# Kernel optimization log

Hardware: AMD Instinct MI355X
Metric: run time of the kernel (lower is better)

Reference implementation:

```python
import jax, jax.numpy as jnp
import numpy as np

NH, HD, WS, LL, SR, HF = 8, 32, 3, 9, 8, 682


def _ln(x, w, b, eps=1e-5):
    m = x.mean(-1, keepdims=True)
    v = ((x - m) ** 2).mean(-1, keepdims=True)
    return (x - m) * jax.lax.rsqrt(v + eps) * w + b


def _l2norm(x, eps=1e-12):
    n = jnp.sqrt(jnp.sum(x * x, axis=-1, keepdims=True))
    return x / jnp.maximum(n, eps)


def setup_inputs() -> dict:
    key = jax.random.key(0)
    ks = jax.random.split(key, 32)
    f32 = jnp.float32
    rn = lambda i, shp, s=0.02: jax.random.normal(ks[i], shp, f32) * s
    B, N, C, T = 8, 3136, 256, 1024
    d = {}
    d['x'] = jax.random.normal(ks[0], (B, N, C), f32)
    d['relative_coords_table'] = jax.random.uniform(ks[1], (T, 2), f32, minval=-1.0, maxval=1.0)
    d['seq_length_scale'] = jnp.ones((1,), f32)
    d['norm1_w'] = jnp.ones((C,), f32); d['norm1_b'] = jnp.zeros((C,), f32)
    d['q_w'] = rn(2, (C, C)); d['q_b'] = rn(3, (C,))
    d['kv_w'] = rn(4, (2 * C, C)); d['kv_b'] = rn(5, (2 * C,))
    d['temperature'] = jnp.full((NH, 1, 1), np.log(np.expm1(1.0 / 0.24)), f32)
    d['query_embedding'] = rn(6, (NH, 1, HD))
    d['relative_pos_bias_local'] = rn(7, (NH, LL), 0.0004)
    d['learnable_tokens'] = rn(8, (NH, HD, LL))
    d['learnable_bias'] = jnp.zeros((NH, 1, LL), f32)
    d['sr_w'] = rn(9, (C, C)); d['sr_b'] = rn(10, (C,))
    d['normp_w'] = jnp.ones((C,), f32); d['normp_b'] = jnp.zeros((C,), f32)
    d['cpb_fc1_w'] = rn(11, (512, 2)); d['cpb_fc1_b'] = rn(12, (512,))
    d['cpb_fc2_w'] = rn(13, (NH, 512)); d['cpb_fc2_b'] = rn(14, (NH,))
    d['proj_w'] = rn(15, (C, C)); d['proj_b'] = rn(16, (C,))
    d['norm2_w'] = jnp.ones((C,), f32); d['norm2_b'] = jnp.zeros((C,), f32)
    d['fc1_w'] = rn(17, (2 * HF, C)); d['fc1_b'] = rn(18, (2 * HF,))
    d['dw_w'] = rn(19, (HF, 1, 3, 3)); d['dw_b'] = rn(20, (HF,))
    d['fc2_w'] = rn(21, (C, HF)); d['fc2_b'] = rn(22, (C,))
    d['relative_pos_index'] = jax.random.randint(ks[23], (N, 49), 0, T)
    d['padding_mask'] = jnp.zeros((N, LL), bool)
    d['H'] = 56
    d['W'] = 56
    return d


def _forward(x, relative_coords_table, seq_length_scale, norm1_w, norm1_b, q_w, q_b, kv_w, kv_b,
             temperature, query_embedding, relative_pos_bias_local, learnable_tokens, learnable_bias,
             sr_w, sr_b, normp_w, normp_b, cpb_fc1_w, cpb_fc1_b, cpb_fc2_w, cpb_fc2_b,
             proj_w, proj_b, norm2_w, norm2_b, fc1_w, fc1_b, dw_w, dw_b, fc2_w, fc2_b,
             relative_pos_index, padding_mask, H, W):
    B, N, C = x.shape
    pH, pW = H // SR, W // SR
    pl = pH * pW
    xn = _ln(x, norm1_w, norm1_b)
    # queries: [B, nh, N, hd], cosine-normalized
    q = (xn @ q_w.T + q_b).reshape(B, N, NH, HD).transpose(0, 2, 1, 3)
    q_norm = _l2norm(q)
    q_scaled = (q_norm + query_embedding) * jax.nn.softplus(temperature) * seq_length_scale
    # local keys/values via unfold (3x3 windows, zero-padded)
    kv = xn @ kv_w.T + kv_b                                   # [B, N, 2C]
    k_l, v_l = jnp.split(kv, 2, axis=-1)
    k_l = _l2norm(k_l.reshape(B, N, NH, HD)).reshape(B, N, C)
    kvl = jnp.concatenate([k_l, v_l], -1).transpose(0, 2, 1).reshape(B, 2 * C, H, W)
    pad = WS // 2
    kvp = jnp.pad(kvl, ((0, 0), (0, 0), (pad, pad), (pad, pad)))
    wins = jnp.stack([kvp[:, :, i:i + H, j:j + W] for i in range(WS) for j in range(WS)], axis=2)
    wins = wins.reshape(B, 2 * NH, HD, LL, N).transpose(0, 1, 4, 2, 3)  # [B, 2nh, N, hd, ll]
    k_loc, v_loc = jnp.split(wins, 2, axis=1)
    attn_local = jnp.einsum('bhnd,bhndl->bhnl', q_scaled, k_loc) + relative_pos_bias_local[None, :, None, :]
    attn_local = jnp.where(padding_mask[None, None], -jnp.inf, attn_local)
    # pooled global branch
    x_ = xn.transpose(0, 2, 1).reshape(B, C, H, W)
    x_ = jax.nn.gelu(jnp.einsum('oc,bchw->bohw', sr_w, x_) + sr_b[None, :, None, None], approximate=False)
    x_ = x_.reshape(B, C, pH, SR, pW, SR).mean(axis=(3, 5))  # adaptive avg pool
    x_ = _ln(x_.reshape(B, C, pl).transpose(0, 2, 1), normp_w, normp_b)
    kvp2 = (x_ @ kv_w.T + kv_b).reshape(B, pl, 2 * NH, HD).transpose(0, 2, 1, 3)
    k_pool, v_pool = jnp.split(kvp2, 2, axis=1)               # [B, nh, pl, hd]
    cpb = jax.nn.relu(relative_coords_table @ cpb_fc1_w.T + cpb_fc1_b) @ cpb_fc2_w.T + cpb_fc2_b
    pool_bias = cpb.T[:, relative_pos_index.reshape(-1)].reshape(NH, N, pl)
    attn_pool = q_scaled @ _l2norm(k_pool).transpose(0, 1, 3, 2) + pool_bias[None]
    # joint softmax over local + pool scores
    attn = jax.nn.softmax(jnp.concatenate([attn_local, attn_pool], -1), axis=-1)
    a_loc, a_pool = attn[..., :LL], attn[..., LL:]
    x_local = jnp.einsum('bhnl,bhndl->bhnd',
                         jnp.einsum('bhnd,hdl->bhnl', q_norm, learnable_tokens) + learnable_bias[None] + a_loc,
                         v_loc)
    x_pool = a_pool @ v_pool
    out = (x_local + x_pool).transpose(0, 2, 1, 3).reshape(B, N, C)
    x = x + (out @ proj_w.T + proj_b)
    # ConvolutionalGLU MLP
    xn2 = _ln(x, norm2_w, norm2_b)
    h = xn2 @ fc1_w.T + fc1_b
    h1, v = jnp.split(h, 2, -1)
    hc = h1.transpose(0, 2, 1).reshape(B, HF, H, W)
    hc = jax.lax.conv_general_dilated(hc, dw_w, (1, 1), 'SAME', feature_group_count=HF,
                                      dimension_numbers=('NCHW', 'OIHW', 'NCHW')) + dw_b[None, :, None, None]
    h1 = hc.reshape(B, HF, N).transpose(0, 2, 1)
    h = jax.nn.gelu(h1, approximate=False) * v
    return x + (h @ fc2_w.T + fc2_b)


def reference(x, relative_coords_table, seq_length_scale, norm1_w, norm1_b, q_w, q_b, kv_w, kv_b,
              temperature, query_embedding, relative_pos_bias_local, learnable_tokens, learnable_bias,
              sr_w, sr_b, normp_w, normp_b, cpb_fc1_w, cpb_fc1_b, cpb_fc2_w, cpb_fc2_b,
              proj_w, proj_b, norm2_w, norm2_b, fc1_w, fc1_b, dw_w, dw_b, fc2_w, fc2_b,
              relative_pos_index, padding_mask, H, W):
    return _forward(x, relative_coords_table, seq_length_scale, norm1_w, norm1_b, q_w, q_b, kv_w, kv_b,
                    temperature, query_embedding, relative_pos_bias_local, learnable_tokens, learnable_bias,
                    sr_w, sr_b, normp_w, normp_b, cpb_fc1_w, cpb_fc1_b, cpb_fc2_w, cpb_fc2_b,
                    proj_w, proj_b, norm2_w, norm2_b, fc1_w, fc1_b, dw_w, dw_b, fc2_w, fc2_b,
                    relative_pos_index, padding_mask, H, W)
```

## Files before the change

kernel.cpp:

```cpp
#include <hip/hip_runtime.h>
#include <math.h>

#define B_   8
#define N_   3136
#define C_   256
#define NH_  8
#define HD_  32
#define LL_  9
#define PL_  49
#define HF_  682
#define HH   56
#define WW   56
#define MROWS (B_*N_)
#define HGLD  704
#define F2LD  704
#define HBLD  1368

typedef short          bf16x8 __attribute__((ext_vector_type(8)));
typedef unsigned short u16x8  __attribute__((ext_vector_type(8)));
typedef float          f32x4  __attribute__((ext_vector_type(4)));
typedef unsigned short u16;

static __device__ __forceinline__ float gelu_f(float x){ return 0.5f*x*(1.0f+erff(x*0.70710678118654752f)); }
static __device__ __forceinline__ u16 f2bf(float f){
  union { float f; unsigned u; } x; x.f = f;
  unsigned r = (x.u + 0x7FFFu + ((x.u >> 16) & 1u)) >> 16;
  return (u16)r;
}
static __device__ __forceinline__ float b2f(u16 u){
  union { unsigned u; float f; } x; x.u = ((unsigned)u) << 16;
  return x.f;
}
static __device__ __forceinline__ void gld_lds16(const u16* g, u16* l){
  __builtin_amdgcn_global_load_lds((const __attribute__((address_space(1))) void*)g,
                                   (__attribute__((address_space(3))) void*)l, 16, 0, 0);
}
static __device__ __forceinline__ float rsum32(float v){
  #pragma unroll
  for (int m=16;m>0;m>>=1) v += __shfl_xor(v,m,32);
  return v;
}
static __device__ __forceinline__ float rsum64(float v){
  #pragma unroll
  for (int m=32;m>0;m>>=1) v += __shfl_xor(v,m,64);
  return v;
}
static __device__ __forceinline__ float rsum8(float v){
  v += __shfl_xor(v,1,64);
  v += __shfl_xor(v,2,64);
  v += __shfl_xor(v,4,64);
  return v;
}

__global__ __launch_bounds__(256) void cvt_all(const float* __restrict__ q_w,
                                               const float* __restrict__ kv_w,
                                               const float* __restrict__ sr_w,
                                               const float* __restrict__ pw,
                                               const float* __restrict__ f1w,
                                               const float* __restrict__ f2w,
                                               const float* __restrict__ lt,
                                               const float* __restrict__ dww,
                                               u16* __restrict__ wq,
                                               u16* __restrict__ wkv,
                                               u16* __restrict__ wsr,
                                               u16* __restrict__ wp,
                                               u16* __restrict__ wf1,
                                               u16* __restrict__ wf2,
                                               u16* __restrict__ w72,
                                               float* __restrict__ dwwT){
  int t = blockIdx.x*256 + threadIdx.x;
  int seg = blockIdx.y;
  const int NT = 64*256;
  if (seg == 0){
    float4 v = *(const float4*)(q_w + (size_t)t*4);
    ushort4 o; o.x=f2bf(v.x); o.y=f2bf(v.y); o.z=f2bf(v.z); o.w=f2bf(v.w);
    *(ushort4*)(wq + (size_t)t*4) = o;
  } else if (seg == 1){
    for (int i=t; i<32768; i+=NT){
      float4 v = *(const float4*)(kv_w + (size_t)i*4);
      ushort4 o; o.x=f2bf(v.x); o.y=f2bf(v.y); o.z=f2bf(v.z); o.w=f2bf(v.w);
      *(ushort4*)(wkv + (size_t)i*4) = o;
    }
  } else if (seg == 2){
    float4 v = *(const float4*)(sr_w + (size_t)t*4);
    ushort4 o; o.x=f2bf(v.x); o.y=f2bf(v.y); o.z=f2bf(v.z); o.w=f2bf(v.w);
    *(ushort4*)(wsr + (size_t)t*4) = o;
  } else if (seg == 3){
    float4 v = *(const float4*)(pw + (size_t)t*4);
    ushort4 o; o.x=f2bf(v.x); o.y=f2bf(v.y); o.z=f2bf(v.z); o.w=f2bf(v.w);
    *(ushort4*)(wp + (size_t)t*4) = o;
  } else if (seg == 4){
    for (int i=t; i<360448; i+=NT){
      int r = i >> 8;
      wf1[i] = (r < 1364) ? f2bf(f1w[i]) : (u16)0;
    }
  } else if (seg == 5){
    for (int i=t; i<256*F2LD; i+=NT){
      int r = i/F2LD, k = i - r*F2LD;
      wf2[i] = (k < HF_) ? f2bf(f2w[(size_t)r*HF_ + k]) : (u16)0;
    }
  } else if (seg == 6){
    for (int i=t; i<72*256; i+=NT){
      int r = i >> 8, c = i & 255;
      int h = r/9, l = r - h*9;
      w72[i] = ((c>>5) == h) ? f2bf(lt[((size_t)(h*32 + (c&31)))*9 + l]) : (u16)0;
    }
  } else {
    for (int i=t; i<9*684; i+=NT){
      int l = i/684, f = i - l*684;
      dwwT[i] = (f < HF_) ? dww[(size_t)f*9 + l] : 0.f;
    }
  }
}

__global__ __launch_bounds__(256) void ln4_kernel(const float* __restrict__ in,
                                                  const float* __restrict__ w,
                                                  const float* __restrict__ bsh,
                                                  u16* __restrict__ out){
  int t = threadIdx.x, wv = t>>6, l = t&63;
  int row = blockIdx.x*4 + wv;
  const float* rp = in + (size_t)row*C_ + l*4;
  float4 v = *(const float4*)rp;
  float s = v.x+v.y+v.z+v.w;
  float q = v.x*v.x+v.y*v.y+v.z*v.z+v.w*v.w;
  s = rsum64(s); q = rsum64(q);
  float m = s*(1.0f/C_);
  float var = q*(1.0f/C_)-m*m;
  float inv = rsqrtf(var+1e-5f);
  float4 wvv = *(const float4*)(w + l*4);
  float4 bvv = *(const float4*)(bsh + l*4);
  ushort4 o;
  o.x = f2bf((v.x-m)*inv*wvv.x + bvv.x);
  o.y = f2bf((v.y-m)*inv*wvv.y + bvv.y);
  o.z = f2bf((v.z-m)*inv*wvv.z + bvv.z);
  o.w = f2bf((v.w-m)*inv*wvv.w + bvv.w);
  *(ushort4*)(out + (size_t)row*C_ + l*4) = o;
}

template<int ACT, int RES, int OUTBF>
__global__ __launch_bounds__(256) void gemm64b(const u16* __restrict__ A, int lda,
                                               const u16* __restrict__ W, int ldw,
                                               const float* __restrict__ bias,
                                               const float* __restrict__ res,
                                               void* __restrict__ outv,
                                               int M, int Nt, int K){
  constexpr int LDT = 40;
  __shared__ u16 As[64*LDT];
  __shared__ u16 Bs[64*LDT];
  int tid = threadIdx.x, lane = tid & 63;
  int wave = tid >> 6;
  int m0 = blockIdx.x*64, n0 = blockIdx.y*64;
  int wm = (wave>>1)*32, wn = (wave&1)*32;
  f32x4 acc[2][2];
  #pragma unroll
  for (int i=0;i<2;i++)
    #pragma unroll
    for (int j=0;j<2;j++) acc[i][j] = (f32x4){0.f,0.f,0.f,0.f};

  const int Kt = (K + 31) & ~31;
  const int l15 = lane & 15, quad = lane >> 4;
  int r  = tid >> 2;
  int c8 = (tid & 3) * 8;

  for (int k0=0; k0<Kt; k0+=32){
    int gk = k0 + c8;
    u16x8 av = (u16x8){0,0,0,0,0,0,0,0};
    if (m0 + r < M && gk + 8 <= lda)
      av = *(const u16x8*)(A + (size_t)(m0+r)*lda + gk);
    *(u16x8*)(&As[r*LDT + c8]) = av;
    u16x8 bv = (u16x8){0,0,0,0,0,0,0,0};
    if (n0 + r < Nt && gk + 8 <= ldw)
      bv = *(const u16x8*)(W + (size_t)(n0+r)*ldw + gk);
    *(u16x8*)(&Bs[r*LDT + c8]) = bv;
    __syncthreads();
    bf16x8 af[2], bfr[2];
    #pragma unroll
    for (int mi=0;mi<2;mi++)
      af[mi] = *(bf16x8*)(&As[(wm + mi*16 + l15)*LDT + quad*8]);
    #pragma unroll
    for (int nj=0;nj<2;nj++)
      bfr[nj] = *(bf16x8*)(&Bs[(wn + nj*16 + l15)*LDT + quad*8]);
    #pragma unroll
    for (int mi=0;mi<2;mi++)
      #pragma unroll
      for (int nj=0;nj<2;nj++)
        acc[mi][nj] = __builtin_amdgcn_mfma_f32_16x16x32_bf16(af[mi], bfr[nj], acc[mi][nj], 0,0,0);
    __syncthreads();
  }
  int rbase = quad*4;
  #pragma unroll
  for (int nj=0;nj<2;nj++){
    int gc = n0 + wn + nj*16 + l15;
    if (gc >= Nt) continue;
    float bv = bias[gc];
    #pragma unroll
    for (int mi=0;mi<2;mi++){
      #pragma unroll
      for (int reg=0;reg<4;reg++){
        int gr = m0 + wm + mi*16 + rbase + reg;
        if (gr >= M) continue;
        float v = acc[mi][nj][reg] + bv;
        if (ACT==1) v = gelu_f(v);
        if (RES)   v += res[(size_t)gr*Nt + gc];
        if (OUTBF) ((u16*)outv)[(size_t)gr*Nt + gc] = f2bf(v);
        else       ((float*)outv)[(size_t)gr*Nt + gc] = v;
      }
    }
  }
}

__global__ __launch_bounds__(256) void gemm64r(const u16* __restrict__ A, int lda,
                                               const u16* __restrict__ W, int ldw,
                                               const float* __restrict__ bias,
                                               const float* __restrict__ res,
                                               float* __restrict__ outv,
                                               int Nt, int Kt){
  constexpr int LDT = 40;
  __shared__ u16 As[64*LDT];
  __shared__ u16 Bs[64*LDT];
  int tid = threadIdx.x, lane = tid & 63;
  int wave = tid >> 6;
  int m0 = blockIdx.x*64, n0 = blockIdx.y*64;
  int wm = (wave>>1)*32, wn = (wave&1)*32;
  f32x4 acc[2][2];
  #pragma unroll
  for (int i=0;i<2;i++)
    #pragma unroll
    for (int j=0;j<2;j++) acc[i][j] = (f32x4){0.f,0.f,0.f,0.f};

  const int l15 = lane & 15, quad = lane >> 4;
  int r  = tid >> 2;
  int c8 = (tid & 3) * 8;
  const u16* ga = A + (size_t)(m0+r)*lda + c8;
  const u16* gb = W + (size_t)(n0+r)*ldw + c8;

  for (int k0=0; k0<Kt; k0+=32){
    *(u16x8*)(&As[r*LDT + c8]) = *(const u16x8*)(ga + k0);
    *(u16x8*)(&Bs[r*LDT + c8]) = *(const u16x8*)(gb + k0);
    __syncthreads();
    bf16x8 af[2], bfr[2];
    #pragma unroll
    for (int mi=0;mi<2;mi++)
      af[mi] = *(bf16x8*)(&As[(wm + mi*16 + l15)*LDT + quad*8]);
    #pragma unroll
    for (int nj=0;nj<2;nj++)
      bfr[nj] = *(bf16x8*)(&Bs[(wn + nj*16 + l15)*LDT + quad*8]);
    #pragma unroll
    for (int mi=0;mi<2;mi++)
      #pragma unroll
      for (int nj=0;nj<2;nj++)
        acc[mi][nj] = __builtin_amdgcn_mfma_f32_16x16x32_bf16(af[mi], bfr[nj], acc[mi][nj], 0,0,0);
    __syncthreads();
  }
  int rbase = quad*4;
  #pragma unroll
  for (int nj=0;nj<2;nj++){
    int gc = n0 + wn + nj*16 + l15;
    float bv = bias[gc];
    #pragma unroll
    for (int mi=0;mi<2;mi++){
      #pragma unroll
      for (int reg=0;reg<4;reg++){
        int gr = m0 + wm + mi*16 + rbase + reg;
        outv[(size_t)gr*Nt + gc] = acc[mi][nj][reg] + bv + res[(size_t)gr*Nt + gc];
      }
    }
  }
}

__global__ __launch_bounds__(256) void gemm64f(const u16* __restrict__ A,
                                               const u16* __restrict__ W0,
                                               const u16* __restrict__ W1,
                                               const u16* __restrict__ W2,
                                               const float* __restrict__ b0,
                                               const float* __restrict__ b1,
                                               const float* __restrict__ b2,
                                               u16* __restrict__ o0,
                                               u16* __restrict__ o1,
                                               u16* __restrict__ o2){
  constexpr int LDT = 40;
  __shared__ u16 As[64*LDT];
  __shared__ u16 Bs[64*LDT];
  int tid = threadIdx.x, lane = tid & 63;
  int wave = tid >> 6;
  int m0 = blockIdx.x*64, y = blockIdx.y;
  const u16* Wp; const float* bp; u16* dst; int dld, dcol0; bool act = false;
  if (y < 4)      { Wp = W0 + (size_t)y*64*C_;      bp = b0 + y*64;      dst = o0; dld = 256; dcol0 = y*64; }
  else if (y < 12){ Wp = W1 + (size_t)(y-4)*64*C_;  bp = b1 + (y-4)*64;  dst = o1; dld = 512; dcol0 = (y-4)*64; }
  else            { Wp = W2 + (size_t)(y-12)*64*C_; bp = b2 + (y-12)*64; dst = o2; dld = 256; dcol0 = (y-12)*64; act = true; }
  int wm = (wave>>1)*32, wn = (wave&1)*32;
  f32x4 acc[2][2];
  #pragma unroll
  for (int i=0;i<2;i++)
    #pragma unroll
    for (int j=0;j<2;j++) acc[i][j] = (f32x4){0.f,0.f,0.f,0.f};

  const int l15 = lane & 15, quad = lane >> 4;
  int r  = tid >> 2;
  int c8 = (tid & 3) * 8;

  #pragma unroll 1
  for (int k0=0; k0<256; k0+=32){
    int gk = k0 + c8;
    *(u16x8*)(&As[r*LDT + c8]) = *(const u16x8*)(A  + (size_t)(m0+r)*C_ + gk);
    *(u16x8*)(&Bs[r*LDT + c8]) = *(const u16x8*)(Wp + (size_t)r*C_ + gk);
    __syncthreads();
    bf16x8 af[2], bfr[2];
    #pragma unroll
    for (int mi=0;mi<2;mi++)
      af[mi] = *(bf16x8*)(&As[(wm + mi*16 + l15)*LDT + quad*8]);
    #pragma unroll
    for (int nj=0;nj<2;nj++)
      bfr[nj] = *(bf16x8*)(&Bs[(wn + nj*16 + l15)*LDT + quad*8]);
    #pragma unroll
    for (int mi=0;mi<2;mi++)
      #pragma unroll
      for (int nj=0;nj<2;nj++)
        acc[mi][nj] = __builtin_amdgcn_mfma_f32_16x16x32_bf16(af[mi], bfr[nj], acc[mi][nj], 0,0,0);
    __syncthreads();
  }
  int rbase = quad*4;
  #pragma unroll
  for (int nj=0;nj<2;nj++){
    int cc = wn + nj*16 + l15;
    float bv = bp[cc];
    #pragma unroll
    for (int mi=0;mi<2;mi++){
      #pragma unroll
      for (int reg=0;reg<4;reg++){
        int gr = m0 + wm + mi*16 + rbase + reg;
        float v = acc[mi][nj][reg] + bv;
        if (act) v = gelu_f(v);
        dst[(size_t)gr*dld + dcol0 + cc] = f2bf(v);
      }
    }
  }
}

template<int EPI>
__global__ __launch_bounds__(256) void gemm128t(const u16* __restrict__ A, int lda,
                                                const u16* __restrict__ W0,
                                                const float* __restrict__ b0,
                                                u16* __restrict__ o0,
                                                int M, int Nt, int K, int ldo){
  __shared__ u16 smem[8704];
  u16* As = smem;
  u16* Bs = smem + 4096;
  int tid = threadIdx.x, lane = tid & 63, wave = tid >> 6;
  int m0 = blockIdx.x*128, y = blockIdx.y;
  int wm = (wave>>1)*64, wn = (wave&1)*64;
  int l15 = lane & 15, quad = lane >> 4;

  const u16* Wp = W0 + (size_t)y*128*(size_t)lda;
  const float* bp = b0;
  u16* dstb = o0; int dld = ldo, dcol0 = y*128;

  f32x4 acc[4][4];
  #pragma unroll
  for (int i=0;i<4;i++)
    #pragma unroll
    for (int j=0;j<4;j++) acc[i][j] = (f32x4){0.f,0.f,0.f,0.f};

  const int Kt = (K + 31) & ~31;
  const u16* ga = A  + (size_t)(m0 + lane)*lda + wave*8;
  const u16* gb = Wp + (size_t)lane*lda + wave*8;
  u16* la = As + wave*1024;
  u16* lb = Bs + wave*1024;

  for (int k0=0; k0<Kt; k0+=32){
    gld_lds16(ga + k0,            la);
    gld_lds16(ga + 64*lda + k0,   la + 512);
    gld_lds16(gb + k0,            lb);
    gld_lds16(gb + 64*lda + k0,   lb + 512);
    __syncthreads();
    bf16x8 af[4], bfr[4];
    #pragma unroll
    for (int mi=0;mi<4;mi++)
      af[mi] = *(bf16x8*)(&As[quad*1024 + (wm + mi*16 + l15)*8]);
    #pragma unroll
    for (int nj=0;nj<4;nj++)
      bfr[nj] = *(bf16x8*)(&Bs[quad*1024 + (wn + nj*16 + l15)*8]);
    #pragma unroll
    for (int mi=0;mi<4;mi++)
      #pragma unroll
      for (int nj=0;nj<4;nj++)
        acc[mi][nj] = __builtin_amdgcn_mfma_f32_16x16x32_bf16(af[mi], bfr[nj], acc[mi][nj], 0,0,0);
    __syncthreads();
  }

  u16* Cs = smem;
  #pragma unroll
  for (int p=0;p<2;p++){
    if (wm == p*64){
      #pragma unroll
      for (int nj=0;nj<4;nj++){
        int cc = wn + nj*16 + l15;
        int gc = dcol0 + cc;
        float bv = (gc < Nt) ? bp[gc] : 0.f;
        #pragma unroll
        for (int mi=0;mi<4;mi++){
          #pragma unroll
          for (int reg=0;reg<4;reg++){
            int rr = mi*16 + quad*4 + reg;
            Cs[rr*136 + cc] = f2bf(acc[mi][nj][reg] + bv);
          }
        }
      }
    }
    __syncthreads();
    int r = tid >> 2, cb = (tid & 3)*32;
    int gr = m0 + p*64 + r;
    if (gr < M){
      u16* op = dstb + (size_t)gr*dld + dcol0;
      #pragma unroll
      for (int k=0;k<4;k++){
        int c0 = cb + k*8;
        if (dcol0 + c0 + 8 <= ldo)
          *(u16x8*)(op + c0) = *(u16x8*)&Cs[r*136 + c0];
      }
    }
    __syncthreads();
  }
}

__global__ __launch_bounds__(256) void post1_kernel(u16* __restrict__ q,
                                                    const float* __restrict__ qe,
                                                    const float* __restrict__ temp,
                                                    const float* __restrict__ sls,
                                                    u16* __restrict__ qs_out,
                                                    u16* __restrict__ kv,
                                                    const u16* __restrict__ xsr,
                                                    const float* __restrict__ npw,
                                                    const float* __restrict__ npb,
                                                    u16* __restrict__ xpln){
  __shared__ float s1[4], s2[4];
  int bid = blockIdx.x, tid = threadIdx.x;
  if (bid < MROWS/4){
    int wv = tid>>6, l = tid&63;
    int row = bid*4 + wv;
    int c = l*4, h = l>>3;
    size_t idx = (size_t)row*C_ + c;
    ushort4 qv = *(const ushort4*)(q + idx);
    float v0=b2f(qv.x), v1=b2f(qv.y), v2=b2f(qv.z), v3=b2f(qv.w);
    float ss = rsum8(v0*v0+v1*v1+v2*v2+v3*v3);
    float inv = 1.0f / fmaxf(sqrtf(ss), 1e-12f);
    float qn0=v0*inv, qn1=v1*inv, qn2=v2*inv, qn3=v3*inv;
    ushort4 qo; qo.x=f2bf(qn0); qo.y=f2bf(qn1); qo.z=f2bf(qn2); qo.w=f2bf(qn3);
    *(ushort4*)(q + idx) = qo;
    float t  = temp[h];
    float sp = log1pf(expf(t));
    float scale = sp * sls[0];
    float4 qev = *(const float4*)(qe + c);
    ushort4 so;
    so.x = f2bf((qn0 + qev.x)*scale);
    so.y = f2bf((qn1 + qev.y)*scale);
    so.z = f2bf((qn2 + qev.z)*scale);
    so.w = f2bf((qn3 + qev.w)*scale);
    *(ushort4*)(qs_out + idx) = so;
    size_t kidx = (size_t)row*512 + c;
    ushort4 kvv = *(const ushort4*)(kv + kidx);
    float k0=b2f(kvv.x), k1=b2f(kvv.y), k2=b2f(kvv.z), k3=b2f(kvv.w);
    float ks = rsum8(k0*k0+k1*k1+k2*k2+k3*k3);
    float kinv = 1.0f / fmaxf(sqrtf(ks), 1e-12f);
    ushort4 ko; ko.x=f2bf(k0*kinv); ko.y=f2bf(k1*kinv); ko.z=f2bf(k2*kinv); ko.w=f2bf(k3*kinv);
    *(ushort4*)(kv + kidx) = ko;
  } else {
    int blk = bid - MROWS/4;
    int b = blk/PL_; int p = blk%PL_;
    int py = p/7, px = p%7;
    int o = tid;
    float s = 0.f;
    for (int iy=0;iy<8;iy++){
      const u16* rowp = xsr + ((size_t)(b*N_ + (py*8+iy)*WW + px*8))*C_ + o;
      #pragma unroll
      for (int ix=0;ix<8;ix++) s += b2f(rowp[(size_t)ix*C_]);
    }
    s *= (1.0f/64.0f);
    float su = rsum64(s), sq = rsum64(s*s);
    if ((o&63)==0){ s1[o>>6]=su; s2[o>>6]=sq; }
    __syncthreads();
    float ts=s1[0]+s1[1]+s1[2]+s1[3];
    float tq=s2[0]+s2[1]+s2[2]+s2[3];
    float m = ts*(1.0f/256.0f), var = tq*(1.0f/256.0f)-m*m;
    float inv = rsqrtf(var+1e-5f);
    xpln[(size_t)blk*C_+o] = f2bf((s-m)*inv*npw[o]+npb[o]);
  }
}

__global__ __launch_bounds__(256) void misc2_kernel(u16* __restrict__ kvp2,
                                                    const float* __restrict__ rct,
                                                    const float* __restrict__ w1,
                                                    const float* __restrict__ b1,
                                                    const float* __restrict__ w2,
                                                    const float* __restrict__ b2v,
                                                    float* __restrict__ cpb){
  __shared__ float r[512];
  int bid = blockIdx.x, tid = threadIdx.x;
  if (bid < B_*PL_){
    int row = bid;
    size_t idx = (size_t)row*512 + tid;
    float v = b2f(kvp2[idx]);
    float ss = rsum32(v*v);
    kvp2[idx] = f2bf(v / fmaxf(sqrtf(ss), 1e-12f));
  } else {
    int t = bid - B_*PL_;
    float c0 = rct[t*2], c1 = rct[t*2+1];
    for (int j=tid;j<512;j+=256){
      float v = c0*w1[j*2] + c1*w1[j*2+1] + b1[j];
      r[j] = fmaxf(v, 0.f);
    }
    __syncthreads();
    int h = tid>>5, lane = tid&31;
    float s = 0.f;
    for (int j=lane;j<512;j+=32) s += r[j]*w2[h*512+j];
    s = rsum32(s);
    if (lane==0) cpb[t*8+h] = s + b2v[h];
  }
}

__global__ __launch_bounds__(256) void attn_all(const u16* __restrict__ qbuf,
                                                const u16* __restrict__ w72,
                                                const float* __restrict__ lb,
                                                float* __restrict__ qlt,
                                                const u16* __restrict__ qs,
                                                const u16* __restrict__ kv,
                                                const float* __restrict__ rpb,
                                                const u16* __restrict__ kvp2,
                                                const float* __restrict__ cpb,
                                                const int* __restrict__ ridx,
                                                float* __restrict__ attn){
  constexpr int LDT = 40;
  __shared__ u16 As[64*LDT];
  __shared__ u16 Bs[64*LDT];
  int bid = blockIdx.x, tid = threadIdx.x;
  int lane = tid & 63, wave = tid >> 6;
  int l15 = lane & 15, quad = lane >> 4;
  if (bid < 784){
    int m0 = (bid % 392)*64, n0 = (bid / 392)*64;
    int wm = (wave>>1)*32, wn = (wave&1)*32;
    f32x4 acc[2][2];
    #pragma unroll
    for (int i=0;i<2;i++)
      #pragma unroll
      for (int j=0;j<2;j++) acc[i][j] = (f32x4){0.f,0.f,0.f,0.f};
    int r  = tid >> 2;
    int c8 = (tid & 3) * 8;
    for (int k0=0; k0<256; k0+=32){
      int gk = k0 + c8;
      *(u16x8*)(&As[r*LDT + c8]) = *(const u16x8*)(qbuf + (size_t)(m0+r)*C_ + gk);
      u16x8 bv = (u16x8){0,0,0,0,0,0,0,0};
      if (n0 + r < 72)
        bv = *(const u16x8*)(w72 + (size_t)(n0+r)*C_ + gk);
      *(u16x8*)(&Bs[r*LDT + c8]) = bv;
      __syncthreads();
      bf16x8 af[2], bfr[2];
      #pragma unroll
      for (int mi=0;mi<2;mi++)
        af[mi] = *(bf16x8*)(&As[(wm + mi*16 + l15)*LDT + quad*8]);
      #pragma unroll
      for (int nj=0;nj<2;nj++)
        bfr[nj] = *(bf16x8*)(&Bs[(wn + nj*16 + l15)*LDT + quad*8]);
      #pragma unroll
      for (int mi=0;mi<2;mi++)
        #pragma unroll
        for (int nj=0;nj<2;nj++)
          acc[mi][nj] = __builtin_amdgcn_mfma_f32_16x16x32_bf16(af[mi], bfr[nj], acc[mi][nj], 0,0,0);
      __syncthreads();
    }
    int rbase = quad*4;
    #pragma unroll
    for (int nj=0;nj<2;nj++){
      int gc = n0 + wn + nj*16 + l15;
      if (gc >= 72) continue;
      float bv = lb[gc];
      #pragma unroll
      for (int mi=0;mi<2;mi++){
        #pragma unroll
        for (int reg=0;reg<4;reg++){
          int gr = m0 + wm + mi*16 + rbase + reg;
          qlt[(size_t)gr*72 + gc] = acc[mi][nj][reg] + bv;
        }
      }
    }
  } else if (bid < 1568){
    int t = tid;
    int row = (bid-784)*32 + (t>>3);
    int h = t & 7;
    int b = row / N_, n = row - b*N_;
    int y = n / WW, x = n - y*WW;
    const u16* qp = qs + (size_t)row*C_ + h*32;
    float q[32];
    #pragma unroll
    for (int j=0;j<4;j++){
      u16x8 v = *(const u16x8*)(qp + j*8);
      #pragma unroll
      for (int e=0;e<8;e++) q[j*8+e] = b2f(v[e]);
    }
    float* arow = attn + ((size_t)row*8 + h)*58;
    #pragma unroll
    for (int l=0;l<9;l++){
      int yy = y + l/3 - 1, xx = x + l%3 - 1;
      float s = 0.f;
      if (yy>=0 && yy<HH && xx>=0 && xx<WW){
        const u16* kp = kv + ((size_t)(b*N_ + yy*WW + xx))*512 + h*32;
        #pragma unroll
        for (int j=0;j<4;j++){
          u16x8 kw = *(const u16x8*)(kp + j*8);
          #pragma unroll
          for (int e=0;e<8;e++) s = fmaf(q[j*8+e], b2f(kw[e]), s);
        }
      }
      arow[l] = s + rpb[h*9+l];
    }
  } else {
    int t = bid - 1568;
    int xblk = t % 49, bh = t / 49;
    int b = bh >> 3, h = bh & 7;
    int n0 = (xblk*4 + wave)*16;
    bf16x8 af = *(const bf16x8*)(qs + ((size_t)(b*N_ + n0 + l15)*C_ + h*32 + quad*8));
    f32x4 acc[4];
    #pragma unroll
    for (int nj=0;nj<4;nj++){
      int p = nj*16 + l15;
      bf16x8 bfr = (bf16x8){0,0,0,0,0,0,0,0};
      if (p < PL_)
        bfr = *(const bf16x8*)(kvp2 + ((size_t)(b*PL_ + p)*512 + h*32 + quad*8));
      f32x4 z = (f32x4){0.f,0.f,0.f,0.f};
      acc[nj] = __builtin_amdgcn_mfma_f32_16x16x32_bf16(af, bfr, z, 0,0,0);
    }
    #pragma unroll
    for (int nj=0;nj<4;nj++){
      int p = nj*16 + l15;
      if (p >= PL_) continue;
      #pragma unroll
      for (int reg=0;reg<4;reg++){
        int n = n0 + quad*4 + reg;
        float bias = cpb[ridx[(size_t)n*PL_ + p]*8 + h];
        attn[((size_t)(b*N_ + n)*8 + h)*58 + 9 + p] = acc[nj][reg] + bias;
      }
    }
  }
}

__global__ __launch_bounds__(256) void xout_v4(const float* __restrict__ qlt,
                                               const float* __restrict__ attn,
                                               const u16* __restrict__ kv,
                                               const u16* __restrict__ kvp2,
                                               u16* __restrict__ out){
  __shared__ float coef[4][472];
  int t = threadIdx.x, w = t>>6, l = t&63;
  int row = blockIdx.x*4 + w;
  int b = row / N_, n = row - b*N_;
  int y = n / WW, x = n - y*WW;
  const float* arow = attn + (size_t)row*464;
  for (int i=l; i<464; i+=64) coef[w][i] = arow[i];
  __syncthreads();
  int h = l>>3, k = l&7;
  float* ch = &coef[w][h*58];
  float e[8];
  float mx = -1e30f;
  #pragma unroll
  for (int i=0;i<8;i++){
    int j = k + i*8;
    e[i] = (j<58) ? ch[j] : -1e30f;
    mx = fmaxf(mx, e[i]);
  }
  mx = fmaxf(mx, __shfl_xor(mx,1,64));
  mx = fmaxf(mx, __shfl_xor(mx,2,64));
  mx = fmaxf(mx, __shfl_xor(mx,4,64));
  float s = 0.f;
  #pragma unroll
  for (int i=0;i<8;i++){
    int j = k + i*8;
    if (j<58){ e[i] = expf(e[i]-mx); s += e[i]; }
  }
  s += __shfl_xor(s,1,64);
  s += __shfl_xor(s,2,64);
  s += __shfl_xor(s,4,64);
  float inv = 1.f/s;
  #pragma unroll
  for (int i=0;i<8;i++){
    int j = k + i*8;
    if (j<58){
      float v = e[i]*inv;
      if (j<9) v += qlt[(size_t)row*72 + h*9 + j];
      ch[j] = v;
    }
  }
  __syncthreads();
  int c = l*4;
  float a0=0.f, a1=0.f, a2=0.f, a3=0.f;
  #pragma unroll
  for (int lw=0; lw<9; lw++){
    int yy = y + lw/3 - 1, xx = x + lw%3 - 1;
    if (yy>=0 && yy<HH && xx>=0 && xx<WW){
      ushort4 vv = *(const ushort4*)(kv + ((size_t)(b*N_ + yy*WW + xx))*512 + 256 + c);
      float cf = ch[lw];
      a0 = fmaf(cf, b2f(vv.x), a0);
      a1 = fmaf(cf, b2f(vv.y), a1);
      a2 = fmaf(cf, b2f(vv.z), a2);
      a3 = fmaf(cf, b2f(vv.w), a3);
    }
  }
  const u16* pb = kvp2 + (size_t)b*PL_*512 + 256 + c;
  #pragma unroll 7
  for (int p=0;p<49;p++){
    ushort4 vv = *(const ushort4*)(pb + (size_t)p*512);
    float cf = ch[9+p];
    a0 = fmaf(cf, b2f(vv.x), a0);
    a1 = fmaf(cf, b2f(vv.y), a1);
    a2 = fmaf(cf, b2f(vv.z), a2);
    a3 = fmaf(cf, b2f(vv.w), a3);
  }
  ushort4 o; o.x=f2bf(a0); o.y=f2bf(a1); o.z=f2bf(a2); o.w=f2bf(a3);
  *(ushort4*)(out + (size_t)row*C_ + c) = o;
}

__global__ __launch_bounds__(256) void dwconv_v4(const u16* __restrict__ hsrc,
                                                 const float* __restrict__ dwwT,
                                                 const float* __restrict__ dwb,
                                                 u16* __restrict__ hg){
  int b = blockIdx.x;
  int idx = blockIdx.y*256 + threadIdx.x;
  if (idx >= N_*86) return;
  int n = idx/86, g = idx - n*86;
  int pix = b*N_ + n;
  int y = n / WW, x = n - y*WW;
  const u16* hb = hsrc + (size_t)b*N_*HBLD;
  if (g < 85){
    int f = g*8;
    float s[8];
    #pragma unroll
    for (int e=0;e<8;e++) s[e] = dwb[f+e];
    #pragma unroll
    for (int l=0;l<9;l++){
      int yy = y + l/3 - 1, xx = x + l%3 - 1;
      if (yy>=0 && yy<HH && xx>=0 && xx<WW){
        u16x8 hv = *(const u16x8*)(hb + (size_t)(yy*WW+xx)*HBLD + f);
        const float* wv = dwwT + (size_t)l*684 + f;
        #pragma unroll
        for (int e=0;e<8;e++) s[e] = fmaf(b2f(hv[e]), wv[e], s[e]);
      }
    }
    const u16* vp = hsrc + (size_t)pix*HBLD + HF_ + f;
    u16 ov[8];
    #pragma unroll
    for (int e=0;e<8;e++) ov[e] = f2bf(gelu_f(s[e]) * b2f(vp[e]));
    *(u16x8*)(hg + (size_t)pix*HGLD + f) = *(u16x8*)ov;
  } else {
    float r[2];
    #pragma unroll
    for (int c=0;c<2;c++){
      int ff = 680 + c;
      float s = dwb[ff];
      #pragma unroll
      for (int l=0;l<9;l++){
        int yy = y + l/3 - 1, xx = x + l%3 - 1;
        if (yy>=0 && yy<HH && xx>=0 && xx<WW)
          s += b2f(hb[(size_t)(yy*WW+xx)*HBLD + ff]) * dwwT[(size_t)l*684 + ff];
      }
      r[c] = gelu_f(s) * b2f(hsrc[(size_t)pix*HBLD + HF_ + ff]);
    }
    u16* hp = hg + (size_t)pix*HGLD;
    ushort4 o1; o1.x = f2bf(r[0]); o1.y = f2bf(r[1]); o1.z = 0; o1.w = 0;
    *(ushort4*)(hp + 680) = o1;
    ushort4 z4 = {0,0,0,0};
    *(ushort4*)(hp + 684) = z4;
    *(ushort4*)(hp + 688) = z4;
    *(ushort4*)(hp + 692) = z4;
    *(ushort4*)(hp + 696) = z4;
    *(ushort4*)(hp + 700) = z4;
  }
}

extern "C" void kernel_launch(void* const* d_in, const int* in_sizes, int n_in,
                              void* d_out, int out_size, void* d_ws, size_t ws_size,
                              hipStream_t stream) {
  const float* x    = (const float*)d_in[0];
  const float* rct  = (const float*)d_in[1];
  const float* sls  = (const float*)d_in[2];
  const float* n1w  = (const float*)d_in[3];
  const float* n1b  = (const float*)d_in[4];
  const float* q_w  = (const float*)d_in[5];
  const float* q_b  = (const float*)d_in[6];
  const float* kv_w = (const float*)d_in[7];
  const float* kv_b = (const float*)d_in[8];
  const float* temp = (const float*)d_in[9];
  const float* qe   = (const float*)d_in[10];
  const float* rpb  = (const float*)d_in[11];
  const float* lt   = (const float*)d_in[12];
  const float* lb   = (const float*)d_in[13];
  const float* sr_w = (const float*)d_in[14];
  const float* sr_b = (const float*)d_in[15];
  const float* npw  = (const float*)d_in[16];
  const float* npb  = (const float*)d_in[17];
  const float* c1w  = (const float*)d_in[18];
  const float* c1b  = (const float*)d_in[19];
  const float* c2w  = (const float*)d_in[20];
  const float* c2b  = (const float*)d_in[21];
  const float* pw   = (const float*)d_in[22];
  const float* pb   = (const float*)d_in[23];
  const float* n2w  = (const float*)d_in[24];
  const float* n2b  = (const float*)d_in[25];
  const float* f1w  = (const float*)d_in[26];
  const float* f1b  = (const float*)d_in[27];
  const float* dww  = (const float*)d_in[28];
  const float* dwb  = (const float*)d_in[29];
  const float* f2w  = (const float*)d_in[30];
  const float* f2bb = (const float*)d_in[31];
  const int*  ridx  = (const int*)d_in[32];
  float* outp = (float*)d_out;

  char* ws = (char*)d_ws;
  constexpr size_t SZ_BNC2 = (size_t)MROWS*C_*2;
  constexpr size_t SZ_KV2  = (size_t)MROWS*512*2;
  constexpr size_t SZ_ATTN = (size_t)MROWS*464*4;
  size_t o_xn   = 0;
  size_t o_qn   = o_xn   + SZ_BNC2;
  size_t o_qs   = o_qn   + SZ_BNC2;
  size_t o_kv   = o_qs   + SZ_BNC2;
  size_t o_attn = o_kv   + SZ_KV2;
  size_t o_xsr  = o_attn + SZ_ATTN;
  size_t o_xpln = o_xsr  + SZ_BNC2;
  size_t o_kvp2 = o_xpln + (size_t)B_*PL_*C_*2;
  size_t o_cpb  = o_kvp2 + (size_t)B_*PL_*512*2;
  size_t o_outb = o_cpb  + (size_t)1024*8*4;
  size_t o_x2   = o_outb + SZ_BNC2;
  size_t o_qlt  = o_x2   + (size_t)MROWS*C_*4;
  size_t o_wq   = o_qlt  + (size_t)MROWS*72*4;
  size_t o_wkv  = o_wq   + (size_t)65536*2;
  size_t o_wsr  = o_wkv  + (size_t)131072*2;
  size_t o_wp   = o_wsr  + (size_t)65536*2;
  size_t o_wf1  = o_wp   + (size_t)65536*2;
  size_t o_wf2  = o_wf1  + (size_t)360448*2;
  size_t o_w72  = o_wf2  + (size_t)256*F2LD*2;
  size_t o_dwwT = o_w72  + (size_t)72*256*2;
  size_t o_h    = o_kv;
  size_t o_hg   = 0;

  u16*   xn   = (u16*)(ws + o_xn);
  u16*   qbuf = (u16*)(ws + o_qn);
  u16*   qsc  = (u16*)(ws + o_qs);
  u16*   kv   = (u16*)(ws + o_kv);
  float* attn = (float*)(ws + o_attn);
  u16*   xsr  = (u16*)(ws + o_xsr);
  u16*   xpln = (u16*)(ws + o_xpln);
  u16*   kvp2 = (u16*)(ws + o_kvp2);
  float* cpb  = (float*)(ws + o_cpb);
  u16*   outb = (u16*)(ws + o_outb);
  float* x2   = (float*)(ws + o_x2);
  float* qlt  = (float*)(ws + o_qlt);
  u16*   wq   = (u16*)(ws + o_wq);
  u16*   wkv  = (u16*)(ws + o_wkv);
  u16*   wsr  = (u16*)(ws + o_wsr);
  u16*   wp   = (u16*)(ws + o_wp);
  u16*   wf1  = (u16*)(ws + o_wf1);
  u16*   wf2  = (u16*)(ws + o_wf2);
  u16*   w72  = (u16*)(ws + o_w72);
  float* dwwT = (float*)(ws + o_dwwT);
  u16*   hbuf = (u16*)(ws + o_h);
  u16*   hg   = (u16*)(ws + o_hg);

  cvt_all<<<dim3(64,8), 256, 0, stream>>>(q_w, kv_w, sr_w, pw, f1w, f2w, lt, dww,
                                          wq, wkv, wsr, wp, wf1, wf2, w72, dwwT);
  ln4_kernel<<<MROWS/4, 256, 0, stream>>>(x, n1w, n1b, xn);
  gemm64f<<<dim3(392,16), 256, 0, stream>>>(xn, wq, wkv, wsr, q_b, kv_b, sr_b,
                                            qbuf, kv, xsr);
  post1_kernel<<<MROWS/4 + B_*PL_, 256, 0, stream>>>(qbuf, qe, temp, sls, qsc, kv,
                                                     xsr, npw, npb, xpln);
  gemm64b<0,0,1><<<dim3(7,8), 256, 0, stream>>>(xpln, C_, wkv, C_, kv_b, nullptr, kvp2, B_*PL_, 512, 256);
  misc2_kernel<<<B_*PL_ + 1024, 256, 0, stream>>>(kvp2, rct, c1w, c1b, c2w, c2b, cpb);
  attn_all<<<784 + 784 + 3136, 256, 0, stream>>>(qbuf, w72, lb, qlt,
                                                 qsc, kv, rpb, kvp2, cpb, ridx, attn);
  xout_v4<<<MROWS/4, 256, 0, stream>>>(qlt, attn, kv, kvp2, outb);
  gemm64r<<<dim3(392,4), 256, 0, stream>>>(outb, C_, wp, C_, pb, x, x2, 256, 256);
  ln4_kernel<<<MROWS/4, 256, 0, stream>>>(x2, n2w, n2b, xn);
  gemm128t<0><<<dim3(196,11), 256, 0, stream>>>(xn, C_, wf1, f1b, hbuf, MROWS, 1364, 256, HBLD);
  dwconv_v4<<<dim3(8, (N_*86+255)/256), 256, 0, stream>>>(hbuf, dwwT, dwb, hg);
  gemm64r<<<dim3(392,4), 256, 0, stream>>>(hg, HGLD, wf2, F2LD, f2bb, x2, outp, 256, 704);
}
```

Before: 503.7 us.

## Fuse local attention logits and learnable-token products into output kernel

Moves the 3x3 local q·k logits and the q·learnable_tokens products out of the big attention kernel and computes them inside the per-row output kernel, where each lane evaluates one or two of the nine local positions. The separate 72-wide MFMA GEMM, its zero-padded block-diagonal weight and the qlt buffer go away. The pooled attention buffer shrinks to 49 entries per head, and the pooled MFMA part now runs as its own kernel. This cuts global writes and re-reads of the logits, but the lane that handles position 8 does twice the work and the dot products run as scalar FMAs instead of MFMA.

```diff
diff --git a/kernel.cpp b/kernel.cpp
--- a/kernel.cpp
+++ b/kernel.cpp
@@ -66,7 +66,7 @@
                                                u16* __restrict__ wp,
                                                u16* __restrict__ wf1,
                                                u16* __restrict__ wf2,
-                                               u16* __restrict__ w72,
+                                               u16* __restrict__ ltT,
                                                float* __restrict__ dwwT){
   int t = blockIdx.x*256 + threadIdx.x;
   int seg = blockIdx.y;
@@ -100,10 +100,10 @@
       wf2[i] = (k < HF_) ? f2bf(f2w[(size_t)r*HF_ + k]) : (u16)0;
     }
   } else if (seg == 6){
-    for (int i=t; i<72*256; i+=NT){
-      int r = i >> 8, c = i & 255;
-      int h = r/9, l = r - h*9;
-      w72[i] = ((c>>5) == h) ? f2bf(lt[((size_t)(h*32 + (c&31)))*9 + l]) : (u16)0;
+    for (int i=t; i<72*32; i+=NT){
+      int r = i >> 5, d = i & 31;
+      int h = r/9, j = r - h*9;
+      ltT[i] = f2bf(lt[((size_t)(h*32 + d))*9 + j]);
     }
   } else {
     for (int i=t; i<9*684; i+=NT){
@@ -518,153 +518,130 @@
   }
 }
 
-__global__ __launch_bounds__(256) void attn_all(const u16* __restrict__ qbuf,
-                                                const u16* __restrict__ w72,
-                                                const float* __restrict__ lb,
-                                                float* __restrict__ qlt,
-                                                const u16* __restrict__ qs,
-                                                const u16* __restrict__ kv,
-                                                const float* __restrict__ rpb,
-                                                const u16* __restrict__ kvp2,
-                                                const float* __restrict__ cpb,
-                                                const int* __restrict__ ridx,
-                                                float* __restrict__ attn){
-  constexpr int LDT = 40;
-  __shared__ u16 As[64*LDT];
-  __shared__ u16 Bs[64*LDT];
-  int bid = blockIdx.x, tid = threadIdx.x;
-  int lane = tid & 63, wave = tid >> 6;
+__global__ __launch_bounds__(256) void attn_pool_mfma(const u16* __restrict__ qs,
+                                                      const u16* __restrict__ kvp2,
+                                                      const float* __restrict__ cpb,
+                                                      const int* __restrict__ ridx,
+                                                      float* __restrict__ attn){
+  int tid = threadIdx.x, lane = tid & 63, wave = tid >> 6;
   int l15 = lane & 15, quad = lane >> 4;
-  if (bid < 784){
-    int m0 = (bid % 392)*64, n0 = (bid / 392)*64;
-    int wm = (wave>>1)*32, wn = (wave&1)*32;
-    f32x4 acc[2][2];
-    #pragma unroll
-    for (int i=0;i<2;i++)
-      #pragma unroll
-      for (int j=0;j<2;j++) acc[i][j] = (f32x4){0.f,0.f,0.f,0.f};
-    int r  = tid >> 2;
-    int c8 = (tid & 3) * 8;
-    for (int k0=0; k0<256; k0+=32){
-      int gk = k0 + c8;
-      *(u16x8*)(&As[r*LDT + c8]) = *(const u16x8*)(qbuf + (size_t)(m0+r)*C_ + gk);
-      u16x8 bv = (u16x8){0,0,0,0,0,0,0,0};
-      if (n0 + r < 72)
-        bv = *(const u16x8*)(w72 + (size_t)(n0+r)*C_ + gk);
-      *(u16x8*)(&Bs[r*LDT + c8]) = bv;
-      __syncthreads();
-      bf16x8 af[2], bfr[2];
-      #pragma unroll
-      for (int mi=0;mi<2;mi++)
-        af[mi] = *(bf16x8*)(&As[(wm + mi*16 + l15)*LDT + quad*8]);
-      #pragma unroll
-      for (int nj=0;nj<2;nj++)
-        bfr[nj] = *(bf16x8*)(&Bs[(wn + nj*16 + l15)*LDT + quad*8]);
-      #pragma unroll
-      for (int mi=0;mi<2;mi++)
-        #pragma unroll
-        for (int nj=0;nj<2;nj++)
-          acc[mi][nj] = __builtin_amdgcn_mfma_f32_16x16x32_bf16(af[mi], bfr[nj], acc[mi][nj], 0,0,0);
-      __syncthreads();
-    }
-    int rbase = quad*4;
-    #pragma unroll
-    for (int nj=0;nj<2;nj++){
-      int gc = n0 + wn + nj*16 + l15;
-      if (gc >= 72) continue;
-      float bv = lb[gc];
-      #pragma unroll
-      for (int mi=0;mi<2;mi++){
-        #pragma unroll
-        for (int reg=0;reg<4;reg++){
-          int gr = m0 + wm + mi*16 + rbase + reg;
-          qlt[(size_t)gr*72 + gc] = acc[mi][nj][reg] + bv;
-        }
-      }
-    }
-  } else if (bid < 1568){
-    int t = tid;
-    int row = (bid-784)*32 + (t>>3);
-    int h = t & 7;
-    int b = row / N_, n = row - b*N_;
-    int y = n / WW, x = n - y*WW;
-    const u16* qp = qs + (size_t)row*C_ + h*32;
-    float q[32];
-    #pragma unroll
-    for (int j=0;j<4;j++){
-      u16x8 v = *(const u16x8*)(qp + j*8);
-      #pragma unroll
-      for (int e=0;e<8;e++) q[j*8+e] = b2f(v[e]);
-    }
-    float* arow = attn + ((size_t)row*8 + h)*58;
-    #pragma unroll
-    for (int l=0;l<9;l++){
-      int yy = y + l/3 - 1, xx = x + l%3 - 1;
-      float s = 0.f;
-      if (yy>=0 && yy<HH && xx>=0 && xx<WW){
-        const u16* kp = kv + ((size_t)(b*N_ + yy*WW + xx))*512 + h*32;
-        #pragma unroll
-        for (int j=0;j<4;j++){
-          u16x8 kw = *(const u16x8*)(kp + j*8);
-          #pragma unroll
-          for (int e=0;e<8;e++) s = fmaf(q[j*8+e], b2f(kw[e]), s);
-        }
-      }
-      arow[l] = s + rpb[h*9+l];
-    }
-  } else {
-    int t = bid - 1568;
-    int xblk = t % 49, bh = t / 49;
-    int b = bh >> 3, h = bh & 7;
-    int n0 = (xblk*4 + wave)*16;
-    bf16x8 af = *(const bf16x8*)(qs + ((size_t)(b*N_ + n0 + l15)*C_ + h*32 + quad*8));
-    f32x4 acc[4];
-    #pragma unroll
-    for (int nj=0;nj<4;nj++){
-      int p = nj*16 + l15;
-      bf16x8 bfr = (bf16x8){0,0,0,0,0,0,0,0};
-      if (p < PL_)
-        bfr = *(const bf16x8*)(kvp2 + ((size_t)(b*PL_ + p)*512 + h*32 + quad*8));
-      f32x4 z = (f32x4){0.f,0.f,0.f,0.f};
-      acc[nj] = __builtin_amdgcn_mfma_f32_16x16x32_bf16(af, bfr, z, 0,0,0);
-    }
-    #pragma unroll
-    for (int nj=0;nj<4;nj++){
-      int p = nj*16 + l15;
-      if (p >= PL_) continue;
-      #pragma unroll
-      for (int reg=0;reg<4;reg++){
-        int n = n0 + quad*4 + reg;
-        float bias = cpb[ridx[(size_t)n*PL_ + p]*8 + h];
-        attn[((size_t)(b*N_ + n)*8 + h)*58 + 9 + p] = acc[nj][reg] + bias;
-      }
-    }
-  }
-}
-
-__global__ __launch_bounds__(256) void xout_v4(const float* __restrict__ qlt,
-                                               const float* __restrict__ attn,
+  int bh = blockIdx.y, b = bh >> 3, h = bh & 7;
+  int n0 = (blockIdx.x*4 + wave)*16;
+  bf16x8 af = *(const bf16x8*)(qs + ((size_t)(b*N_ + n0 + l15)*C_ + h*32 + quad*8));
+  f32x4 acc[4];
+  #pragma unroll
+  for (int nj=0;nj<4;nj++){
+    int p = nj*16 + l15;
+    bf16x8 bfr = (bf16x8){0,0,0,0,0,0,0,0};
+    if (p < PL_)
+      bfr = *(const bf16x8*)(kvp2 + ((size_t)(b*PL_ + p)*512 + h*32 + quad*8));
+    f32x4 z = (f32x4){0.f,0.f,0.f,0.f};
+    acc[nj] = __builtin_amdgcn_mfma_f32_16x16x32_bf16(af, bfr, z, 0,0,0);
+  }
+  #pragma unroll
+  for (int nj=0;nj<4;nj++){
+    int p = nj*16 + l15;
+    if (p >= PL_) continue;
+    #pragma unroll
+    for (int reg=0;reg<4;reg++){
+      int n = n0 + quad*4 + reg;
+      float bias = cpb[ridx[(size_t)n*PL_ + p]*8 + h];
+      attn[(size_t)(b*N_ + n)*392 + h*49 + p] = acc[nj][reg] + bias;
+    }
+  }
+}
+
+__global__ __launch_bounds__(256) void xout_v6(const u16* __restrict__ qn,
+                                               const u16* __restrict__ qsc,
+                                               const float* __restrict__ attnp,
                                                const u16* __restrict__ kv,
                                                const u16* __restrict__ kvp2,
+                                               const float* __restrict__ rpb,
+                                               const u16* __restrict__ ltT,
+                                               const float* __restrict__ lb,
                                                u16* __restrict__ out){
   __shared__ float coef[4][472];
   int t = threadIdx.x, w = t>>6, l = t&63;
   int row = blockIdx.x*4 + w;
   int b = row / N_, n = row - b*N_;
   int y = n / WW, x = n - y*WW;
-  const float* arow = attn + (size_t)row*464;
-  for (int i=l; i<464; i+=64) coef[w][i] = arow[i];
+  const float* arow = attnp + (size_t)row*392;
+  for (int i=l; i<392; i+=64){
+    int h2 = i/49, p = i - h2*49;
+    coef[w][h2*58 + 9 + p] = arow[i];
+  }
+  int h = l>>3, k = l&7;
+  float qs_[32], qn_[32];
+  const u16* qsp = qsc + (size_t)row*C_ + h*32;
+  const u16* qnp = qn  + (size_t)row*C_ + h*32;
+  #pragma unroll
+  for (int j=0;j<4;j++){
+    u16x8 v1 = *(const u16x8*)(qsp + j*8);
+    u16x8 v2 = *(const u16x8*)(qnp + j*8);
+    #pragma unroll
+    for (int e8=0;e8<8;e8++){ qs_[j*8+e8] = b2f(v1[e8]); qn_[j*8+e8] = b2f(v2[e8]); }
+  }
+  float e0, e1loc = 0.f, ql0, ql1 = 0.f;
+  {
+    int j = k;
+    int yy = y + j/3 - 1, xx = x + j%3 - 1;
+    float s = 0.f;
+    if (yy>=0 && yy<HH && xx>=0 && xx<WW){
+      const u16* kp = kv + ((size_t)(b*N_ + yy*WW + xx))*512 + h*32;
+      #pragma unroll
+      for (int jj=0;jj<4;jj++){
+        u16x8 kw = *(const u16x8*)(kp + jj*8);
+        #pragma unroll
+        for (int ee=0;ee<8;ee++) s = fmaf(qs_[jj*8+ee], b2f(kw[ee]), s);
+      }
+    }
+    e0 = s + rpb[h*9+j];
+    float d = lb[h*9+j];
+    const u16* lp = ltT + (size_t)(h*9+j)*32;
+    #pragma unroll
+    for (int jj=0;jj<4;jj++){
+      u16x8 lw = *(const u16x8*)(lp + jj*8);
+      #pragma unroll
+      for (int ee=0;ee<8;ee++) d = fmaf(qn_[jj*8+ee], b2f(lw[ee]), d);
+    }
+    ql0 = d;
+  }
+  if (k == 0){
+    int yy = y + 1, xx = x + 1;
+    float s = 0.f;
+    if (yy < HH && xx < WW){
+      const u16* kp = kv + ((size_t)(b*N_ + yy*WW + xx))*512 + h*32;
+      #pragma unroll
+      for (int jj=0;jj<4;jj++){
+        u16x8 kw = *(const u16x8*)(kp + jj*8);
+        #pragma unroll
+        for (int ee=0;ee<8;ee++) s = fmaf(qs_[jj*8+ee], b2f(kw[ee]), s);
+      }
+    }
+    e1loc = s + rpb[h*9+8];
+    float d = lb[h*9+8];
+    const u16* lp = ltT + (size_t)(h*9+8)*32;
+    #pragma unroll
+    for (int jj=0;jj<4;jj++){
+      u16x8 lw = *(const u16x8*)(lp + jj*8);
+      #pragma unroll
+      for (int ee=0;ee<8;ee++) d = fmaf(qn_[jj*8+ee], b2f(lw[ee]), d);
+    }
+    ql1 = d;
+  }
   __syncthreads();
-  int h = l>>3, k = l&7;
   float* ch = &coef[w][h*58];
   float e[8];
-  float mx = -1e30f;
-  #pragma unroll
-  for (int i=0;i<8;i++){
+  e[0] = e0;
+  e[1] = (k==0) ? e1loc : ch[k+8];
+  #pragma unroll
+  for (int i=2;i<8;i++){
     int j = k + i*8;
     e[i] = (j<58) ? ch[j] : -1e30f;
-    mx = fmaxf(mx, e[i]);
-  }
+  }
+  float mx = -1e30f;
+  #pragma unroll
+  for (int i=0;i<8;i++) mx = fmaxf(mx, e[i]);
   mx = fmaxf(mx, __shfl_xor(mx,1,64));
   mx = fmaxf(mx, __shfl_xor(mx,2,64));
   mx = fmaxf(mx, __shfl_xor(mx,4,64));
@@ -683,7 +660,8 @@
     int j = k + i*8;
     if (j<58){
       float v = e[i]*inv;
-      if (j<9) v += qlt[(size_t)row*72 + h*9 + j];
+      if (i==0) v += ql0;
+      if (i==1 && k==0) v += ql1;
       ch[j] = v;
     }
   }
@@ -849,20 +827,19 @@
   float* cpb  = (float*)(ws + o_cpb);
   u16*   outb = (u16*)(ws + o_outb);
   float* x2   = (float*)(ws + o_x2);
-  float* qlt  = (float*)(ws + o_qlt);
   u16*   wq   = (u16*)(ws + o_wq);
   u16*   wkv  = (u16*)(ws + o_wkv);
   u16*   wsr  = (u16*)(ws + o_wsr);
   u16*   wp   = (u16*)(ws + o_wp);
   u16*   wf1  = (u16*)(ws + o_wf1);
   u16*   wf2  = (u16*)(ws + o_wf2);
-  u16*   w72  = (u16*)(ws + o_w72);
+  u16*   ltT  = (u16*)(ws + o_w72);
   float* dwwT = (float*)(ws + o_dwwT);
   u16*   hbuf = (u16*)(ws + o_h);
   u16*   hg   = (u16*)(ws + o_hg);
 
   cvt_all<<<dim3(64,8), 256, 0, stream>>>(q_w, kv_w, sr_w, pw, f1w, f2w, lt, dww,
-                                          wq, wkv, wsr, wp, wf1, wf2, w72, dwwT);
+                                          wq, wkv, wsr, wp, wf1, wf2, ltT, dwwT);
   ln4_kernel<<<MROWS/4, 256, 0, stream>>>(x, n1w, n1b, xn);
   gemm64f<<<dim3(392,16), 256, 0, stream>>>(xn, wq, wkv, wsr, q_b, kv_b, sr_b,
                                             qbuf, kv, xsr);
@@ -870,9 +847,8 @@
                                                      xsr, npw, npb, xpln);
   gemm64b<0,0,1><<<dim3(7,8), 256, 0, stream>>>(xpln, C_, wkv, C_, kv_b, nullptr, kvp2, B_*PL_, 512, 256);
   misc2_kernel<<<B_*PL_ + 1024, 256, 0, stream>>>(kvp2, rct, c1w, c1b, c2w, c2b, cpb);
-  attn_all<<<784 + 784 + 3136, 256, 0, stream>>>(qbuf, w72, lb, qlt,
-                                                 qsc, kv, rpb, kvp2, cpb, ridx, attn);
-  xout_v4<<<MROWS/4, 256, 0, stream>>>(qlt, attn, kv, kvp2, outb);
+  attn_pool_mfma<<<dim3(49,64), 256, 0, stream>>>(qsc, kvp2, cpb, ridx, attn);
+  xout_v6<<<MROWS/4, 256, 0, stream>>>(qbuf, qsc, attn, kv, kvp2, rpb, ltT, lb, outb);
   gemm64r<<<dim3(392,4), 256, 0, stream>>>(outb, C_, wp, C_, pb, x, x2, 256, 256);
   ln4_kernel<<<MROWS/4, 256, 0, stream>>>(x2, n2w, n2b, xn);
   gemm128t<0><<<dim3(196,11), 256, 0, stream>>>(xn, C_, wf1, f1b, hbuf, MROWS, 1364, 256, HBLD);
```

Measured after the change: 513.2 us. About the same (+1.9%).
